# Performance work log

Hardware: AMD Instinct MI355X
Metric: run time of the kernel (lower is better)

## Reference

```python
import jax, jax.numpy as jnp
import numpy as np
import math

N_DRUG, N_DIS, D, EMB, HEADS, STEPS = 3072, 3072, 64, 16, 4, 5
N = N_DRUG + N_DIS


def setup_inputs() -> dict:
    key = jax.random.key(0)
    ks = jax.random.split(key, 16)
    s = lambda fan: 1.0 / np.sqrt(fan)
    return {
        "graph": jax.random.uniform(ks[0], (N, N), jnp.float32),
        "drug_f": jax.random.normal(ks[1], (N_DRUG, D), jnp.float32),
        "disease_f": jax.random.normal(ks[2], (N_DIS, D), jnp.float32),
        "timesteps": jax.random.randint(ks[3], (N,), 0, STEPS, jnp.int32),
        "drug_w": jax.random.normal(ks[4], (D, D), jnp.float32) * s(D),
        "disease_w": jax.random.normal(ks[5], (D, D), jnp.float32) * s(D),
        "emb_w": jax.random.normal(ks[6], (EMB, EMB), jnp.float32) * s(EMB),
        "emb_b": jnp.zeros((EMB,), jnp.float32),
        "in_w": jax.random.normal(ks[7], (D + EMB, 256), jnp.float32) * s(D + EMB),
        "in_b": jnp.zeros((256,), jnp.float32),
        "out_w": jax.random.normal(ks[8], (256, D), jnp.float32) * s(256),
        "out_b": jnp.zeros((D,), jnp.float32),
        "wq": jax.random.normal(ks[9], (D, D), jnp.float32) * s(D),
        "bq": jnp.zeros((D,), jnp.float32),
        "wk": jax.random.normal(ks[10], (D, D), jnp.float32) * s(D),
        "bk": jnp.zeros((D,), jnp.float32),
        "wv": jax.random.normal(ks[11], (D, D), jnp.float32) * s(D),
        "bv": jnp.zeros((D,), jnp.float32),
        "wo": jax.random.normal(ks[12], (D, D), jnp.float32) * s(D),
        "bo": jnp.zeros((D,), jnp.float32),
        "fuse_w": jax.random.normal(ks[13], (2 * D, D), jnp.float32) * s(2 * D),
        "fuse_b": jnp.zeros((D,), jnp.float32),
        "ln_g": jnp.ones((D,), jnp.float32),
        "ln_b": jnp.zeros((D,), jnp.float32),
    }


def _layernorm(x, g, b, eps=1e-5):
    mu = jnp.mean(x, axis=-1, keepdims=True)
    var = jnp.var(x, axis=-1, keepdims=True)
    return (x - mu) * jax.lax.rsqrt(var + eps) * g + b


def reference(graph, drug_f, disease_f, timesteps, drug_w, disease_w,
              emb_w, emb_b, in_w, in_b, out_w, out_b,
              wq, bq, wk, bk, wv, bv, wo, bo,
              fuse_w, fuse_b, ln_g, ln_b):
    # ---- DGLLayer: per-type projection + symmetric degree-norm propagation ----
    node_f = jnp.concatenate([drug_f @ drug_w, disease_f @ disease_w], axis=0)  # [N, D]
    degs = jnp.clip(jnp.sum(graph, axis=1), 1.0, None)
    norm = jax.lax.rsqrt(degs)[:, None]  # degs^-0.5, [N, 1]
    target = (graph @ (node_f * norm)) * norm

    # ---- Denoise MLP with sinusoidal time embedding ----
    half = EMB // 2
    freqs = jnp.exp(-math.log(10000.0) * jnp.arange(half, dtype=jnp.float32) / half)
    temp = timesteps.astype(jnp.float32)[:, None] * freqs[None]  # [N, half]
    time_emb = jnp.concatenate([jnp.cos(temp), jnp.sin(temp)], axis=-1)  # [N, EMB]
    emb = time_emb @ emb_w + emb_b
    h = jnp.concatenate([target, emb], axis=-1)  # [N, D+EMB]
    h = jnp.tanh(h @ in_w + in_b)  # in-layer
    aux = h @ out_w + out_b        # final out-layer (no tanh)

    # ---- AttentionFusion: cross-attention(target -> aux) + fuse + residual LN ----
    hd = D // HEADS
    q = (target @ wq + bq).reshape(N, HEADS, hd)
    k = (aux @ wk + bk).reshape(N, HEADS, hd)
    v = (aux @ wv + bv).reshape(N, HEADS, hd)
    scores = jnp.einsum('nhd,mhd->hnm', q, k) / np.sqrt(hd)  # [H, N, N]
    attn = jax.nn.softmax(scores, axis=-1)
    attn_out = jnp.einsum('hnm,mhd->nhd', attn, v).reshape(N, D) @ wo + bo
    fused = jnp.concatenate([target, attn_out], axis=-1) @ fuse_w + fuse_b
    return _layernorm(fused + target, ln_g, ln_b)
```

## Files before the change

kernel.cpp:

```cpp
#include <hip/hip_runtime.h>
#include <cstdint>
#include <cstddef>

#define NTOT 6144
#define NDRUG 3072
#define NM (NTOT*64)

typedef __fp16 f16;
typedef __attribute__((ext_vector_type(2))) __fp16 f16x2;
typedef __attribute__((ext_vector_type(4))) __fp16 f16x4;
typedef __attribute__((ext_vector_type(8))) __fp16 f16x8;
typedef __attribute__((ext_vector_type(4))) float f32x4;

__device__ __forceinline__ f16x8 pack8(float4 a, float4 b){
  f16x2 p0 = __builtin_amdgcn_cvt_pkrtz(a.x, a.y);
  f16x2 p1 = __builtin_amdgcn_cvt_pkrtz(a.z, a.w);
  f16x2 p2 = __builtin_amdgcn_cvt_pkrtz(b.x, b.y);
  f16x2 p3 = __builtin_amdgcn_cvt_pkrtz(b.z, b.w);
  f16x4 lo = __builtin_shufflevector(p0, p1, 0, 1, 2, 3);
  f16x4 hi = __builtin_shufflevector(p2, p3, 0, 1, 2, 3);
  return __builtin_shufflevector(lo, hi, 0, 1, 2, 3, 4, 5, 6, 7);
}

__global__ __launch_bounds__(256) void k_deg(const float* __restrict__ g,
                                             const float* __restrict__ drug_f,
                                             const float* __restrict__ dis_f,
                                             const float* __restrict__ drug_w,
                                             const float* __restrict__ dis_w,
                                             float* __restrict__ norm,
                                             float* __restrict__ nfs){
  __shared__ float sx[4][64];
  int wv = threadIdx.x >> 6, j = threadIdx.x & 63;
  int row = blockIdx.x*4 + wv;
  const float4* p = (const float4*)(g + (size_t)row * NTOT);
  float s = 0.f;
  #pragma unroll
  for (int it = 0; it < 24; ++it) {
    float4 u = p[it*64 + j];
    s += u.x + u.y + u.z + u.w;
  }
  #pragma unroll
  for (int off = 32; off; off >>= 1) s += __shfl_xor(s, off, 64);
  float nrm = rsqrtf(fmaxf(s, 1.0f));
  if (j == 0) norm[row] = nrm;

  const float* x; const float* W;
  if (row < NDRUG){ x = drug_f + (size_t)row*64; W = drug_w; }
  else            { x = dis_f + (size_t)(row-NDRUG)*64; W = dis_w; }
  sx[wv][j] = x[j];
  __syncthreads();
  float acc = 0.f;
  #pragma unroll 8
  for (int k = 0; k < 64; ++k) acc = fmaf(sx[wv][k], W[k*64+j], acc);
  nfs[(size_t)row*64 + j] = acc * nrm;
}

__global__ __launch_bounds__(256) void k_gemm(const float* __restrict__ graph,
                                              const float* __restrict__ nfs,
                                              float* __restrict__ part){
  __shared__ f16 sA[64][72];
  __shared__ f16 sBt[64][72];
  const int tid = threadIdx.x;
  const int lane = tid & 63, w = tid >> 6;
  const int l15 = lane & 15, quad = lane >> 4;
  const int row0 = blockIdx.x * 64;
  const int kbase = blockIdx.y * 768;

  f32x4 acc[4] = {{0.f,0.f,0.f,0.f},{0.f,0.f,0.f,0.f},
                  {0.f,0.f,0.f,0.f},{0.f,0.f,0.f,0.f}};

  const int ar = tid >> 2, acg = (tid & 3) * 16;
  const int bk = (tid & 31) * 2, bng = (tid >> 5) * 8;

  for (int kt = 0; kt < 12; ++kt){
    const int k0 = kbase + kt*64;
    __syncthreads();
    {
      const float4* srcA = (const float4*)(graph + (size_t)(row0 + ar)*NTOT + k0 + acg);
      float4 a0 = srcA[0], a1 = srcA[1], a2 = srcA[2], a3 = srcA[3];
      *(f16x8*)&sA[ar][acg]     = pack8(a0, a1);
      *(f16x8*)&sA[ar][acg + 8] = pack8(a2, a3);
      const float4* b0p = (const float4*)(nfs + (size_t)(k0 + bk)*64 + bng);
      const float4* b1p = (const float4*)(nfs + (size_t)(k0 + bk + 1)*64 + bng);
      float4 r00 = b0p[0], r01 = b0p[1];
      float4 r10 = b1p[0], r11 = b1p[1];
      float e0[8] = {r00.x,r00.y,r00.z,r00.w,r01.x,r01.y,r01.z,r01.w};
      float e1[8] = {r10.x,r10.y,r10.z,r10.w,r11.x,r11.y,r11.z,r11.w};
      #pragma unroll
      for (int i = 0; i < 8; ++i){
        f16x2 pr = __builtin_amdgcn_cvt_pkrtz(e0[i], e1[i]);
        *(f16x2*)&sBt[bng + i][bk] = pr;
      }
    }
    __syncthreads();
    #pragma unroll
    for (int k16 = 0; k16 < 4; ++k16){
      f16x4 af = *(const f16x4*)&sA[w*16 + l15][k16*16 + quad*4];
      #pragma unroll
      for (int nt = 0; nt < 4; ++nt){
        f16x4 bf = *(const f16x4*)&sBt[nt*16 + l15][k16*16 + quad*4];
        acc[nt] = __builtin_amdgcn_mfma_f32_16x16x16f16(af, bf, acc[nt], 0, 0, 0);
      }
    }
  }
  float* dst = part + (size_t)blockIdx.y * NM;
  #pragma unroll
  for (int nt = 0; nt < 4; ++nt){
    #pragma unroll
    for (int r = 0; r < 4; ++r){
      int row = row0 + w*16 + quad*4 + r;
      dst[(size_t)row*64 + nt*16 + l15] = acc[nt][r];
    }
  }
}

__global__ __launch_bounds__(256) void k_node2(const float* __restrict__ part,
                                               const float* __restrict__ norm,
                                               const int* __restrict__ ts,
                                               const float* __restrict__ emb_w,
                                               const float* __restrict__ emb_b,
                                               const float* __restrict__ in_w,
                                               const float* __restrict__ in_b,
                                               const float* __restrict__ out_w,
                                               const float* __restrict__ out_b,
                                               const float* __restrict__ wq, const float* __restrict__ bq,
                                               const float* __restrict__ wk, const float* __restrict__ bk,
                                               const float* __restrict__ wvw, const float* __restrict__ bv,
                                               float* __restrict__ target,
                                               float* __restrict__ qb, float* __restrict__ kb,
                                               float* __restrict__ vb){
  __shared__ float sx[4][80];
  __shared__ float sh[4][256];
  __shared__ float sa[4][64];
  int wv = threadIdx.x>>6, j = threadIdx.x&63;
  int row = blockIdx.x*4 + wv;

  float t = 0.f;
  #pragma unroll
  for (int p = 0; p < 8; ++p) t += part[(size_t)p*NM + (size_t)row*64 + j];
  t *= norm[row];
  target[(size_t)row*64 + j] = t;
  sx[wv][j] = t;
  if (j < 16) {
    const float FREQ[8] = {1.0f, 0.316227766016838f, 0.1f, 0.0316227766016838f,
                           0.01f, 0.00316227766016838f, 0.001f, 0.000316227766016838f};
    float tt = (float)ts[row];
    float e = emb_b[j];
    #pragma unroll
    for (int k = 0; k < 8; ++k) {
      float a = tt * FREQ[k];
      e = fmaf(cosf(a), emb_w[k*16 + j], e);
      e = fmaf(sinf(a), emb_w[(8+k)*16 + j], e);
    }
    sx[wv][64 + j] = e;
  }
  __syncthreads();
  float a0 = in_b[4*j+0], a1 = in_b[4*j+1], a2 = in_b[4*j+2], a3 = in_b[4*j+3];
  #pragma unroll 8
  for (int k = 0; k < 80; ++k) {
    float xv = sx[wv][k];
    float4 w = *(const float4*)(in_w + k*256 + 4*j);
    a0 = fmaf(xv, w.x, a0);
    a1 = fmaf(xv, w.y, a1);
    a2 = fmaf(xv, w.z, a2);
    a3 = fmaf(xv, w.w, a3);
  }
  sh[wv][4*j+0] = tanhf(a0); sh[wv][4*j+1] = tanhf(a1);
  sh[wv][4*j+2] = tanhf(a2); sh[wv][4*j+3] = tanhf(a3);
  __syncthreads();
  float o = out_b[j];
  #pragma unroll 8
  for (int k = 0; k < 256; ++k) o = fmaf(sh[wv][k], out_w[k*64 + j], o);
  sa[wv][j] = o;
  __syncthreads();
  float q = bq[j], kk = bk[j], vv = bv[j];
  #pragma unroll 8
  for (int k = 0; k < 64; ++k) {
    float tv = sx[wv][k], av = sa[wv][k];
    q  = fmaf(tv, wq[k*64+j],  q);
    kk = fmaf(av, wk[k*64+j],  kk);
    vv = fmaf(av, wvw[k*64+j], vv);
  }
  qb[(size_t)row*64+j]=q; kb[(size_t)row*64+j]=kk; vb[(size_t)row*64+j]=vv;
}

__global__ __launch_bounds__(256) void k_attn(const float* __restrict__ qb,
                                              const float* __restrict__ kb,
                                              const float* __restrict__ vb,
                                              float* __restrict__ pattn){
  __shared__ f16 sK[64][72];
  __shared__ f16 sVt[64][72];
  const int tid = threadIdx.x;
  const int h = tid >> 6;
  const int lane = tid & 63;
  const int l15 = lane & 15, quad = lane >> 4;
  const int z = blockIdx.y;
  const int q0 = blockIdx.x * 64;

  f16x4 qf[4];
  #pragma unroll
  for (int qn = 0; qn < 4; ++qn){
    float4 v = *(const float4*)(qb + (size_t)(q0 + qn*16 + l15)*64 + h*16 + quad*4);
    f16x2 lo = __builtin_amdgcn_cvt_pkrtz(v.x, v.y);
    f16x2 hi = __builtin_amdgcn_cvt_pkrtz(v.z, v.w);
    qf[qn] = __builtin_shufflevector(lo, hi, 0, 1, 2, 3);
  }

  f32x4 accOT[4] = {{0.f,0.f,0.f,0.f},{0.f,0.f,0.f,0.f},
                    {0.f,0.f,0.f,0.f},{0.f,0.f,0.f,0.f}};
  float lsum[4] = {0.f, 0.f, 0.f, 0.f};

  const int kr = tid >> 2, kdc = (tid & 3) * 16;
  const int vk = (tid & 31) * 2, vdg = (tid >> 5) * 8;

  const int kbase = z * 768;
  for (int kt = 0; kt < 12; ++kt){
    const int k0 = kbase + kt*64;
    __syncthreads();
    {
      const float4* srcK = (const float4*)(kb + (size_t)(k0 + kr)*64 + kdc);
      float4 ka = srcK[0], kbv = srcK[1], kc = srcK[2], kd = srcK[3];
      *(f16x8*)&sK[kr][kdc]     = pack8(ka, kbv);
      *(f16x8*)&sK[kr][kdc + 8] = pack8(kc, kd);
      const float4* v0p = (const float4*)(vb + (size_t)(k0 + vk)*64 + vdg);
      const float4* v1p = (const float4*)(vb + (size_t)(k0 + vk + 1)*64 + vdg);
      float4 r00 = v0p[0], r01 = v0p[1];
      float4 r10 = v1p[0], r11 = v1p[1];
      float e0[8] = {r00.x,r00.y,r00.z,r00.w,r01.x,r01.y,r01.z,r01.w};
      float e1[8] = {r10.x,r10.y,r10.z,r10.w,r11.x,r11.y,r11.z,r11.w};
      #pragma unroll
      for (int i = 0; i < 8; ++i){
        f16x2 pr = __builtin_amdgcn_cvt_pkrtz(e0[i], e1[i]);
        *(f16x2*)&sVt[vdg + i][vk] = pr;
      }
    }
    __syncthreads();
    #pragma unroll
    for (int km = 0; km < 4; ++km){
      f16x4 kf = *(const f16x4*)&sK[km*16 + l15][h*16 + quad*4];
      f16x4 vf = *(const f16x4*)&sVt[h*16 + l15][km*16 + quad*4];
      #pragma unroll
      for (int qn = 0; qn < 4; ++qn){
        f32x4 s = __builtin_amdgcn_mfma_f32_16x16x16f16(
            kf, qf[qn], (f32x4){0.f,0.f,0.f,0.f}, 0, 0, 0);
        float p0 = __expf(fminf(s[0]*0.25f, 10.f));
        float p1 = __expf(fminf(s[1]*0.25f, 10.f));
        float p2 = __expf(fminf(s[2]*0.25f, 10.f));
        float p3 = __expf(fminf(s[3]*0.25f, 10.f));
        lsum[qn] += (p0 + p1) + (p2 + p3);
        f16x2 plo = __builtin_amdgcn_cvt_pkrtz(p0, p1);
        f16x2 phi = __builtin_amdgcn_cvt_pkrtz(p2, p3);
        f16x4 pf = __builtin_shufflevector(plo, phi, 0, 1, 2, 3);
        accOT[qn] = __builtin_amdgcn_mfma_f32_16x16x16f16(vf, pf, accOT[qn], 0, 0, 0);
      }
    }
  }
  #pragma unroll
  for (int qn = 0; qn < 4; ++qn){
    lsum[qn] += __shfl_xor(lsum[qn], 16, 64);
    lsum[qn] += __shfl_xor(lsum[qn], 32, 64);
  }
  #pragma unroll
  for (int qn = 0; qn < 4; ++qn){
    float* rec = pattn + ((size_t)(z*4 + h)*NTOT + q0 + qn*16 + l15) * 20;
    *(float4*)(rec + quad*4) =
        make_float4(accOT[qn][0], accOT[qn][1], accOT[qn][2], accOT[qn][3]);
    if (quad == 0){ rec[17] = lsum[qn]; }
  }
}

__global__ __launch_bounds__(256) void k_out(const float* __restrict__ pattn,
                                             const float* __restrict__ target,
                                             const float* __restrict__ wo, const float* __restrict__ bo,
                                             const float* __restrict__ fuse_w, const float* __restrict__ fuse_b,
                                             const float* __restrict__ ln_g, const float* __restrict__ ln_b,
                                             float* __restrict__ out){
  __shared__ float st[4][64], sa[4][64], sao[4][64];
  int wv = threadIdx.x>>6, j = threadIdx.x&63;
  int row = blockIdx.x*4 + wv;
  int h = j >> 4, d = j & 15;
  float osum = 0.f, L = 0.f;
  #pragma unroll
  for (int z = 0; z < 8; ++z) {
    const float* rec = pattn + ((size_t)(z*4 + h)*NTOT + row)*20;
    osum += rec[d];
    L += rec[17];
  }
  sa[wv][j] = osum / L;
  st[wv][j] = target[(size_t)row*64+j];
  __syncthreads();
  float ao = bo[j];
  #pragma unroll 8
  for (int k = 0; k < 64; ++k) ao = fmaf(sa[wv][k], wo[k*64+j], ao);
  sao[wv][j] = ao;
  __syncthreads();
  float f = fuse_b[j];
  #pragma unroll 8
  for (int k = 0; k < 64; ++k) f = fmaf(st[wv][k], fuse_w[k*64+j], f);
  #pragma unroll 8
  for (int k = 0; k < 64; ++k) f = fmaf(sao[wv][k], fuse_w[(64+k)*64+j], f);
  float x = f + st[wv][j];
  float s1 = x, s2 = x*x;
  #pragma unroll
  for (int off = 32; off; off >>= 1) { s1 += __shfl_xor(s1, off, 64); s2 += __shfl_xor(s2, off, 64); }
  float mu = s1*(1.f/64.f);
  float var = s2*(1.f/64.f) - mu*mu;
  float y = (x-mu)*rsqrtf(var + 1e-5f)*ln_g[j] + ln_b[j];
  out[(size_t)row*64 + j] = y;
}

extern "C" void kernel_launch(void* const* d_in, const int* in_sizes, int n_in,
                              void* d_out, int out_size, void* d_ws, size_t ws_size,
                              hipStream_t stream) {
  const float* graph  = (const float*)d_in[0];
  const float* drug_f = (const float*)d_in[1];
  const float* dis_f  = (const float*)d_in[2];
  const int*   ts     = (const int*)d_in[3];
  const float* drug_w = (const float*)d_in[4];
  const float* dis_w  = (const float*)d_in[5];
  const float* emb_w  = (const float*)d_in[6];
  const float* emb_b  = (const float*)d_in[7];
  const float* in_w   = (const float*)d_in[8];
  const float* in_b   = (const float*)d_in[9];
  const float* out_w  = (const float*)d_in[10];
  const float* out_b  = (const float*)d_in[11];
  const float* wq     = (const float*)d_in[12];
  const float* bq     = (const float*)d_in[13];
  const float* wk     = (const float*)d_in[14];
  const float* bk     = (const float*)d_in[15];
  const float* wvw    = (const float*)d_in[16];
  const float* bv     = (const float*)d_in[17];
  const float* wo     = (const float*)d_in[18];
  const float* bo     = (const float*)d_in[19];
  const float* fuse_w = (const float*)d_in[20];
  const float* fuse_b = (const float*)d_in[21];
  const float* ln_g   = (const float*)d_in[22];
  const float* ln_b   = (const float*)d_in[23];

  float* ws     = (float*)d_ws;
  float* norm   = ws;
  float* nfs    = norm + 8192;
  float* target = nfs + NM;
  float* qb     = target + NM;
  float* kb     = qb + NM;
  float* vb     = kb + NM;
  float* part   = vb + NM;
  float* pattn  = part + (size_t)8*NM;

  k_deg<<<1536, 256, 0, stream>>>(graph, drug_f, dis_f, drug_w, dis_w, norm, nfs);
  k_gemm<<<dim3(96, 8), 256, 0, stream>>>(graph, nfs, part);
  k_node2<<<1536, 256, 0, stream>>>(part, norm, ts, emb_w, emb_b, in_w, in_b,
                                    out_w, out_b, wq, bq, wk, bk, wvw, bv,
                                    target, qb, kb, vb);
  k_attn<<<dim3(96, 8), 256, 0, stream>>>(qb, kb, vb, pattn);
  k_out<<<1536, 256, 0, stream>>>(pattn, target, wo, bo, fuse_w, fuse_b,
                                  ln_g, ln_b, (float*)d_out);
}
```

Before: 402.2 us.

## Pre-convert graph and operands to fp16 layouts and double-buffer GEMM/attention tiles

The degree kernel now also writes an fp16 copy of the adjacency matrix and a transposed fp16 copy of the normalized features. The propagation GEMM can then load half-width, already-transposed tiles with no per-tile conversion. The node kernel likewise emits fp16 Q (pre-scaled by 1/sqrt(hd)), fp16 K and transposed fp16 V, and both the GEMM and attention kernels use register-staged double-buffered shared-memory tiles. This trades extra write traffic in the first kernel (a half-size graph copy) for fewer bytes and less conversion work in the GEMM, and adds overlap of global loads with MFMA work.

```diff
diff --git a/kernel.cpp b/kernel.cpp
--- a/kernel.cpp
+++ b/kernel.cpp
@@ -7,20 +7,9 @@
 #define NM (NTOT*64)
 
 typedef __fp16 f16;
-typedef __attribute__((ext_vector_type(2))) __fp16 f16x2;
 typedef __attribute__((ext_vector_type(4))) __fp16 f16x4;
 typedef __attribute__((ext_vector_type(8))) __fp16 f16x8;
 typedef __attribute__((ext_vector_type(4))) float f32x4;
-
-__device__ __forceinline__ f16x8 pack8(float4 a, float4 b){
-  f16x2 p0 = __builtin_amdgcn_cvt_pkrtz(a.x, a.y);
-  f16x2 p1 = __builtin_amdgcn_cvt_pkrtz(a.z, a.w);
-  f16x2 p2 = __builtin_amdgcn_cvt_pkrtz(b.x, b.y);
-  f16x2 p3 = __builtin_amdgcn_cvt_pkrtz(b.z, b.w);
-  f16x4 lo = __builtin_shufflevector(p0, p1, 0, 1, 2, 3);
-  f16x4 hi = __builtin_shufflevector(p2, p3, 0, 1, 2, 3);
-  return __builtin_shufflevector(lo, hi, 0, 1, 2, 3, 4, 5, 6, 7);
-}
 
 __global__ __launch_bounds__(256) void k_deg(const float* __restrict__ g,
                                              const float* __restrict__ drug_f,
@@ -28,16 +17,21 @@
                                              const float* __restrict__ drug_w,
                                              const float* __restrict__ dis_w,
                                              float* __restrict__ norm,
-                                             float* __restrict__ nfs){
+                                             f16* __restrict__ gh,
+                                             f16* __restrict__ nfst){
   __shared__ float sx[4][64];
+  __shared__ float snf[4][64];
   int wv = threadIdx.x >> 6, j = threadIdx.x & 63;
   int row = blockIdx.x*4 + wv;
   const float4* p = (const float4*)(g + (size_t)row * NTOT);
+  f16* ghrow = gh + (size_t)row * NTOT;
   float s = 0.f;
   #pragma unroll
   for (int it = 0; it < 24; ++it) {
     float4 u = p[it*64 + j];
-    s += u.x + u.y + u.z + u.w;
+    s += (u.x + u.y) + (u.z + u.w);
+    f16x4 pk = {(f16)u.x, (f16)u.y, (f16)u.z, (f16)u.w};
+    *(f16x4*)(ghrow + (size_t)(it*64 + j)*4) = pk;
   }
   #pragma unroll
   for (int off = 32; off; off >>= 1) s += __shfl_xor(s, off, 64);
@@ -52,56 +46,58 @@
   float acc = 0.f;
   #pragma unroll 8
   for (int k = 0; k < 64; ++k) acc = fmaf(sx[wv][k], W[k*64+j], acc);
-  nfs[(size_t)row*64 + j] = acc * nrm;
-}
-
-__global__ __launch_bounds__(256) void k_gemm(const float* __restrict__ graph,
-                                              const float* __restrict__ nfs,
+  snf[wv][j] = acc * nrm;
+  __syncthreads();
+  if (threadIdx.x < 64){
+    int c = threadIdx.x;
+    f16x4 pk = {(f16)snf[0][c], (f16)snf[1][c], (f16)snf[2][c], (f16)snf[3][c]};
+    *(f16x4*)(nfst + (size_t)c*NTOT + blockIdx.x*4) = pk;
+  }
+}
+
+__global__ __launch_bounds__(256) void k_gemm(const f16* __restrict__ gh,
+                                              const f16* __restrict__ nfst,
                                               float* __restrict__ part){
-  __shared__ f16 sA[64][72];
-  __shared__ f16 sBt[64][72];
+  __shared__ f16 sA[2][64][72];
+  __shared__ f16 sB[2][64][72];
   const int tid = threadIdx.x;
   const int lane = tid & 63, w = tid >> 6;
   const int l15 = lane & 15, quad = lane >> 4;
   const int row0 = blockIdx.x * 64;
   const int kbase = blockIdx.y * 768;
+  const int sr = tid >> 2, scg = (tid & 3) * 16;
 
   f32x4 acc[4] = {{0.f,0.f,0.f,0.f},{0.f,0.f,0.f,0.f},
                   {0.f,0.f,0.f,0.f},{0.f,0.f,0.f,0.f}};
-
-  const int ar = tid >> 2, acg = (tid & 3) * 16;
-  const int bk = (tid & 31) * 2, bng = (tid >> 5) * 8;
-
+  f16x8 ra0, ra1, rb0, rb1;
+  auto LOADT = [&](int kt){
+    const f16* pa = gh + (size_t)(row0 + sr)*NTOT + kbase + kt*64 + scg;
+    ra0 = *(const f16x8*)pa; ra1 = *(const f16x8*)(pa + 8);
+    const f16* pb = nfst + (size_t)sr*NTOT + kbase + kt*64 + scg;
+    rb0 = *(const f16x8*)pb; rb1 = *(const f16x8*)(pb + 8);
+  };
+  auto WRITET = [&](int b){
+    *(f16x8*)&sA[b][sr][scg]     = ra0;
+    *(f16x8*)&sA[b][sr][scg + 8] = ra1;
+    *(f16x8*)&sB[b][sr][scg]     = rb0;
+    *(f16x8*)&sB[b][sr][scg + 8] = rb1;
+  };
+  LOADT(0); WRITET(0);
+  int cur = 0;
   for (int kt = 0; kt < 12; ++kt){
-    const int k0 = kbase + kt*64;
-    __syncthreads();
-    {
-      const float4* srcA = (const float4*)(graph + (size_t)(row0 + ar)*NTOT + k0 + acg);
-      float4 a0 = srcA[0], a1 = srcA[1], a2 = srcA[2], a3 = srcA[3];
-      *(f16x8*)&sA[ar][acg]     = pack8(a0, a1);
-      *(f16x8*)&sA[ar][acg + 8] = pack8(a2, a3);
-      const float4* b0p = (const float4*)(nfs + (size_t)(k0 + bk)*64 + bng);
-      const float4* b1p = (const float4*)(nfs + (size_t)(k0 + bk + 1)*64 + bng);
-      float4 r00 = b0p[0], r01 = b0p[1];
-      float4 r10 = b1p[0], r11 = b1p[1];
-      float e0[8] = {r00.x,r00.y,r00.z,r00.w,r01.x,r01.y,r01.z,r01.w};
-      float e1[8] = {r10.x,r10.y,r10.z,r10.w,r11.x,r11.y,r11.z,r11.w};
-      #pragma unroll
-      for (int i = 0; i < 8; ++i){
-        f16x2 pr = __builtin_amdgcn_cvt_pkrtz(e0[i], e1[i]);
-        *(f16x2*)&sBt[bng + i][bk] = pr;
-      }
-    }
+    if (kt < 11) LOADT(kt + 1);
     __syncthreads();
     #pragma unroll
     for (int k16 = 0; k16 < 4; ++k16){
-      f16x4 af = *(const f16x4*)&sA[w*16 + l15][k16*16 + quad*4];
+      f16x4 af = *(const f16x4*)&sA[cur][w*16 + l15][k16*16 + quad*4];
       #pragma unroll
       for (int nt = 0; nt < 4; ++nt){
-        f16x4 bf = *(const f16x4*)&sBt[nt*16 + l15][k16*16 + quad*4];
+        f16x4 bf = *(const f16x4*)&sB[cur][nt*16 + l15][k16*16 + quad*4];
         acc[nt] = __builtin_amdgcn_mfma_f32_16x16x16f16(af, bf, acc[nt], 0, 0, 0);
       }
     }
+    if (kt < 11) WRITET(cur ^ 1);
+    cur ^= 1;
   }
   float* dst = part + (size_t)blockIdx.y * NM;
   #pragma unroll
@@ -127,11 +123,12 @@
                                                const float* __restrict__ wk, const float* __restrict__ bk,
                                                const float* __restrict__ wvw, const float* __restrict__ bv,
                                                float* __restrict__ target,
-                                               float* __restrict__ qb, float* __restrict__ kb,
-                                               float* __restrict__ vb){
+                                               f16* __restrict__ qh, f16* __restrict__ kh,
+                                               f16* __restrict__ vt){
   __shared__ float sx[4][80];
   __shared__ float sh[4][256];
   __shared__ float sa[4][64];
+  __shared__ float sv[4][64];
   int wv = threadIdx.x>>6, j = threadIdx.x&63;
   int row = blockIdx.x*4 + wv;
 
@@ -181,15 +178,23 @@
     kk = fmaf(av, wk[k*64+j],  kk);
     vv = fmaf(av, wvw[k*64+j], vv);
   }
-  qb[(size_t)row*64+j]=q; kb[(size_t)row*64+j]=kk; vb[(size_t)row*64+j]=vv;
-}
-
-__global__ __launch_bounds__(256) void k_attn(const float* __restrict__ qb,
-                                              const float* __restrict__ kb,
-                                              const float* __restrict__ vb,
+  qh[(size_t)row*64+j] = (f16)(q * 0.25f);
+  kh[(size_t)row*64+j] = (f16)kk;
+  sv[wv][j] = vv;
+  __syncthreads();
+  if (threadIdx.x < 64){
+    int c = threadIdx.x;
+    f16x4 pk = {(f16)sv[0][c], (f16)sv[1][c], (f16)sv[2][c], (f16)sv[3][c]};
+    *(f16x4*)(vt + (size_t)c*NTOT + blockIdx.x*4) = pk;
+  }
+}
+
+__global__ __launch_bounds__(256) void k_attn(const f16* __restrict__ qh,
+                                              const f16* __restrict__ kh,
+                                              const f16* __restrict__ vt,
                                               float* __restrict__ pattn){
-  __shared__ f16 sK[64][72];
-  __shared__ f16 sVt[64][72];
+  __shared__ f16 sK[2][64][72];
+  __shared__ f16 sV[2][64][72];
   const int tid = threadIdx.x;
   const int h = tid >> 6;
   const int lane = tid & 63;
@@ -199,61 +204,53 @@
 
   f16x4 qf[4];
   #pragma unroll
-  for (int qn = 0; qn < 4; ++qn){
-    float4 v = *(const float4*)(qb + (size_t)(q0 + qn*16 + l15)*64 + h*16 + quad*4);
-    f16x2 lo = __builtin_amdgcn_cvt_pkrtz(v.x, v.y);
-    f16x2 hi = __builtin_amdgcn_cvt_pkrtz(v.z, v.w);
-    qf[qn] = __builtin_shufflevector(lo, hi, 0, 1, 2, 3);
-  }
+  for (int qn = 0; qn < 4; ++qn)
+    qf[qn] = *(const f16x4*)(qh + (size_t)(q0 + qn*16 + l15)*64 + h*16 + quad*4);
 
   f32x4 accOT[4] = {{0.f,0.f,0.f,0.f},{0.f,0.f,0.f,0.f},
                     {0.f,0.f,0.f,0.f},{0.f,0.f,0.f,0.f}};
   float lsum[4] = {0.f, 0.f, 0.f, 0.f};
-
-  const int kr = tid >> 2, kdc = (tid & 3) * 16;
-  const int vk = (tid & 31) * 2, vdg = (tid >> 5) * 8;
-
+  const int sr = tid >> 2, scg = (tid & 3) * 16;
   const int kbase = z * 768;
+  f16x8 rk0, rk1, rv0, rv1;
+  auto LOADT = [&](int kt){
+    const int k0 = kbase + kt*64;
+    const f16* pk = kh + (size_t)(k0 + sr)*64 + scg;
+    rk0 = *(const f16x8*)pk; rk1 = *(const f16x8*)(pk + 8);
+    const f16* pv = vt + (size_t)sr*NTOT + k0 + scg;
+    rv0 = *(const f16x8*)pv; rv1 = *(const f16x8*)(pv + 8);
+  };
+  auto WRITET = [&](int b){
+    *(f16x8*)&sK[b][sr][scg]     = rk0;
+    *(f16x8*)&sK[b][sr][scg + 8] = rk1;
+    *(f16x8*)&sV[b][sr][scg]     = rv0;
+    *(f16x8*)&sV[b][sr][scg + 8] = rv1;
+  };
+  LOADT(0); WRITET(0);
+  int cur = 0;
   for (int kt = 0; kt < 12; ++kt){
-    const int k0 = kbase + kt*64;
-    __syncthreads();
-    {
-      const float4* srcK = (const float4*)(kb + (size_t)(k0 + kr)*64 + kdc);
-      float4 ka = srcK[0], kbv = srcK[1], kc = srcK[2], kd = srcK[3];
-      *(f16x8*)&sK[kr][kdc]     = pack8(ka, kbv);
-      *(f16x8*)&sK[kr][kdc + 8] = pack8(kc, kd);
-      const float4* v0p = (const float4*)(vb + (size_t)(k0 + vk)*64 + vdg);
-      const float4* v1p = (const float4*)(vb + (size_t)(k0 + vk + 1)*64 + vdg);
-      float4 r00 = v0p[0], r01 = v0p[1];
-      float4 r10 = v1p[0], r11 = v1p[1];
-      float e0[8] = {r00.x,r00.y,r00.z,r00.w,r01.x,r01.y,r01.z,r01.w};
-      float e1[8] = {r10.x,r10.y,r10.z,r10.w,r11.x,r11.y,r11.z,r11.w};
-      #pragma unroll
-      for (int i = 0; i < 8; ++i){
-        f16x2 pr = __builtin_amdgcn_cvt_pkrtz(e0[i], e1[i]);
-        *(f16x2*)&sVt[vdg + i][vk] = pr;
-      }
-    }
+    if (kt < 11) LOADT(kt + 1);
     __syncthreads();
     #pragma unroll
     for (int km = 0; km < 4; ++km){
-      f16x4 kf = *(const f16x4*)&sK[km*16 + l15][h*16 + quad*4];
-      f16x4 vf = *(const f16x4*)&sVt[h*16 + l15][km*16 + quad*4];
+      f16x4 kf = *(const f16x4*)&sK[cur][km*16 + l15][h*16 + quad*4];
+      f16x4 vf = *(const f16x4*)&sV[cur][h*16 + l15][km*16 + quad*4];
       #pragma unroll
       for (int qn = 0; qn < 4; ++qn){
         f32x4 s = __builtin_amdgcn_mfma_f32_16x16x16f16(
             kf, qf[qn], (f32x4){0.f,0.f,0.f,0.f}, 0, 0, 0);
-        float p0 = __expf(fminf(s[0]*0.25f, 10.f));
-        float p1 = __expf(fminf(s[1]*0.25f, 10.f));
-        float p2 = __expf(fminf(s[2]*0.25f, 10.f));
-        float p3 = __expf(fminf(s[3]*0.25f, 10.f));
+        float p0 = __expf(fminf(s[0], 10.f));
+        float p1 = __expf(fminf(s[1], 10.f));
+        float p2 = __expf(fminf(s[2], 10.f));
+        float p3 = __expf(fminf(s[3], 10.f));
         lsum[qn] += (p0 + p1) + (p2 + p3);
-        f16x2 plo = __builtin_amdgcn_cvt_pkrtz(p0, p1);
-        f16x2 phi = __builtin_amdgcn_cvt_pkrtz(p2, p3);
-        f16x4 pf = __builtin_shufflevector(plo, phi, 0, 1, 2, 3);
+        f16x4 pf;
+        pf[0] = (f16)p0; pf[1] = (f16)p1; pf[2] = (f16)p2; pf[3] = (f16)p3;
         accOT[qn] = __builtin_amdgcn_mfma_f32_16x16x16f16(vf, pf, accOT[qn], 0, 0, 0);
       }
     }
+    if (kt < 11) WRITET(cur ^ 1);
+    cur ^= 1;
   }
   #pragma unroll
   for (int qn = 0; qn < 4; ++qn){
@@ -339,20 +336,22 @@
 
   float* ws     = (float*)d_ws;
   float* norm   = ws;
-  float* nfs    = norm + 8192;
-  float* target = nfs + NM;
-  float* qb     = target + NM;
-  float* kb     = qb + NM;
-  float* vb     = kb + NM;
-  float* part   = vb + NM;
+  f16*   gh     = (f16*)(ws + 8192);
+  float* base   = ws + 8192 + (size_t)NTOT*NTOT/2;
+  f16*   nfst   = (f16*)base;
+  float* target = base + (size_t)64*NTOT/2;
+  f16*   qh     = (f16*)(target + NM);
+  f16*   kh     = (f16*)(target + NM + NM/2);
+  f16*   vt     = (f16*)(target + NM + NM);
+  float* part   = target + NM + NM + NM/2;
   float* pattn  = part + (size_t)8*NM;
 
-  k_deg<<<1536, 256, 0, stream>>>(graph, drug_f, dis_f, drug_w, dis_w, norm, nfs);
-  k_gemm<<<dim3(96, 8), 256, 0, stream>>>(graph, nfs, part);
+  k_deg<<<1536, 256, 0, stream>>>(graph, drug_f, dis_f, drug_w, dis_w, norm, gh, nfst);
+  k_gemm<<<dim3(96, 8), 256, 0, stream>>>(gh, nfst, part);
   k_node2<<<1536, 256, 0, stream>>>(part, norm, ts, emb_w, emb_b, in_w, in_b,
                                     out_w, out_b, wq, bq, wk, bk, wvw, bv,
-                                    target, qb, kb, vb);
-  k_attn<<<dim3(96, 8), 256, 0, stream>>>(qb, kb, vb, pattn);
+                                    target, qh, kh, vt);
+  k_attn<<<dim3(96, 8), 256, 0, stream>>>(qh, kh, vt, pattn);
   k_out<<<1536, 256, 0, stream>>>(pattn, target, wo, bo, fuse_w, fuse_b,
                                   ln_g, ln_b, (float*)d_out);
 }
```

Measured after the change: 399.0 us. About the same (-0.8%).
